# Kernel tuning notes

Hardware: AMD Instinct MI355X
Metric: run time of the kernel (lower is better)

## Reference

```python
import jax, jax.numpy as jnp
import numpy as np

D_MODEL = 1024
D_FF = 4096
N_EXPERTS = 8
TOP_K = 2
B, S = 4, 2048


def setup_inputs() -> dict:
    key = jax.random.key(0)
    ks = jax.random.split(key, 8)
    std = 0.02
    x = jax.random.normal(ks[0], (B, S, D_MODEL), dtype=jnp.float32)
    router_w = jax.random.normal(ks[1], (N_EXPERTS, D_MODEL), dtype=jnp.float32) * std
    router_b = jnp.zeros((N_EXPERTS,), dtype=jnp.float32)
    # stacked expert FFN weights (torch Linear layout: [out, in])
    w1 = jax.random.normal(ks[2], (N_EXPERTS, D_FF, D_MODEL), dtype=jnp.float32) * std
    b1 = jnp.zeros((N_EXPERTS, D_FF), dtype=jnp.float32)
    w2 = jax.random.normal(ks[3], (N_EXPERTS, D_MODEL, D_FF), dtype=jnp.float32) * std
    b2 = jnp.zeros((N_EXPERTS, D_MODEL), dtype=jnp.float32)
    return {"x": x, "router_w": router_w, "router_b": router_b,
            "w1": w1, "b1": b1, "w2": w2, "b2": b2}


def reference(x, router_w, router_b, w1, b1, w2, b2):
    Bx, Sx, D = x.shape
    E = router_b.shape[0]
    xf = x.reshape(-1, D)                                  # [T, D]
    logits = xf @ router_w.T + router_b                    # [T, E]
    probs = jax.nn.softmax(logits, axis=-1)
    topk_w, topk_idx = jax.lax.top_k(probs, TOP_K)         # [T, K]
    topk_w = topk_w / jnp.sum(topk_w, axis=-1, keepdims=True)
    # dense per-token/per-expert combine weights (zero for unselected experts)
    onehot = jax.nn.one_hot(topk_idx, E, dtype=xf.dtype)   # [T, K, E]
    w_dense = jnp.einsum('tke,tk->te', onehot, topk_w)     # [T, E]
    out = jnp.zeros_like(xf)
    for e in range(E):  # small fixed loop over experts (unrolled under jit)
        h = jax.nn.gelu(xf @ w1[e].T + b1[e], approximate=False)  # [T, F]
        out = out + w_dense[:, e:e + 1] * (h @ w2[e].T + b2[e])
    return out.reshape(Bx, Sx, D)
```

## Files before the change

### kernel.cpp

```cpp
#include <hip/hip_runtime.h>
#include <stdint.h>

typedef unsigned short u16;
typedef __bf16 bf16x8 __attribute__((ext_vector_type(8)));
typedef float f32x4 __attribute__((ext_vector_type(4)));

#define T_TOK 8192
#define DM    1024
#define DF    4096
#define NE    8
#define BM    128
#define BK    64
#define MAXT  136


__device__ __forceinline__ u16 f2b(float f) {
  union { float f; uint32_t u; } v; v.f = f;
  uint32_t r = (v.u + 0x7FFFu + ((v.u >> 16) & 1u)) >> 16;
  return (u16)r;
}

__device__ __forceinline__ void async16(const void* g, void* l) {
  __builtin_amdgcn_global_load_lds((const __attribute__((address_space(1))) void*)g,
                                   (__attribute__((address_space(3))) void*)l, 16, 0, 0);
}

__device__ __forceinline__ float fast_gelu(float v) {
  float x = v * 0.70710678118654752f;
  float a = fabsf(x);
  float t = __builtin_amdgcn_rcpf(fmaf(0.3275911f, a, 1.0f));
  float p = t * fmaf(t, fmaf(t, fmaf(t, fmaf(t, 1.061405429f, -1.453152027f),
                                     1.421413741f), -0.284496736f), 0.254829592f);
  float e = __expf(-a * a);
  float erf_a = fmaf(-p, e, 1.0f);
  float erf_x = (x < 0.f) ? -erf_a : erf_a;
  return 0.5f * v * (1.0f + erf_x);
}


__global__ __launch_bounds__(256) void router_k(
    const float* __restrict__ x, const float* __restrict__ rw,
    const float* __restrict__ rb, u16* __restrict__ xb,
    float* __restrict__ wsl, int* __restrict__ bucket, int* __restrict__ counts)
{
  int lane = threadIdx.x & 63;
  int t = blockIdx.x * 4 + (threadIdx.x >> 6);
  const float* xp = x + (size_t)t * DM;
  float acc[NE];
#pragma unroll
  for (int e = 0; e < NE; ++e) acc[e] = 0.f;
  for (int i = 0; i < DM / 64; ++i) {
    int idx = i * 64 + lane;
    float xv = xp[idx];
    xb[(size_t)t * DM + idx] = f2b(xv);
#pragma unroll
    for (int e = 0; e < NE; ++e) acc[e] += xv * rw[e * DM + idx];
  }
#pragma unroll
  for (int e = 0; e < NE; ++e) {
#pragma unroll
    for (int off = 32; off >= 1; off >>= 1) acc[e] += __shfl_xor(acc[e], off);
  }
  if (lane == 0) {
    float l[NE];
#pragma unroll
    for (int e = 0; e < NE; ++e) l[e] = acc[e] + rb[e];
    int i1 = 0;
#pragma unroll
    for (int e = 1; e < NE; ++e) if (l[e] > l[i1]) i1 = e;
    int i2 = (i1 == 0) ? 1 : 0;
#pragma unroll
    for (int e = 0; e < NE; ++e) if (e != i1 && l[e] > l[i2]) i2 = e;
    float e2 = expf(l[i2] - l[i1]);
    float wa = 1.f / (1.f + e2);
    wsl[2 * t]     = wa;
    wsl[2 * t + 1] = 1.f - wa;
    int p1 = atomicAdd(&counts[i1], 1); bucket[i1 * T_TOK + p1] = 2 * t;
    int p2 = atomicAdd(&counts[i2], 1); bucket[i2 * T_TOK + p2] = 2 * t + 1;
  }
}


struct alignas(8) U16x4 { u16 x, y, z, w; };

__global__ __launch_bounds__(256) void cvt_k(const float* __restrict__ w,
                                             u16* __restrict__ o)
{
  int i = blockIdx.x * 256 + threadIdx.x;
  float4 v = ((const float4*)w)[i];
  U16x4 u; u.x = f2b(v.x); u.y = f2b(v.y); u.z = f2b(v.z); u.w = f2b(v.w);
  ((U16x4*)o)[i] = u;
}


__global__ void toff_k(const int* __restrict__ counts, int* __restrict__ toff) {
  if (threadIdx.x == 0 && blockIdx.x == 0) {
    int a = 0;
    for (int e = 0; e < NE; ++e) { toff[e] = a; a += (counts[e] + BM - 1) >> 7; }
    toff[NE] = a;
  }
}


__global__ __launch_bounds__(256, 2) void stage1_k(
    const u16* __restrict__ xb, const u16* __restrict__ w1b,
    const float* __restrict__ b1, const int* __restrict__ bucket,
    const int* __restrict__ counts, const int* __restrict__ toff,
    u16* __restrict__ H)
{
  __shared__ __align__(16) u16 sA[BM * BK];
  __shared__ __align__(16) u16 sB[BM * BK];
  __shared__ int sSlot[BM];

  int bid = blockIdx.y * 32 + blockIdx.x;
  int lid = (bid & 7) * ((32 * MAXT) >> 3) + (bid >> 3);
  int fs = lid & 31;
  int tb = lid >> 5;
  if (tb >= toff[NE]) return;
  int e = 0;
#pragma unroll
  for (int q = 1; q < NE; ++q) if (tb >= toff[q]) e = q;
  int ti = tb - toff[e];
  int cnt = counts[e];
  int tid = threadIdx.x;

  if (tid < BM) {
    int r = ti * BM + tid;
    sSlot[tid] = (r < cnt) ? bucket[e * T_TOK + r] : -1;
  }
  __syncthreads();

  int tokA[4];
#pragma unroll
  for (int c = 0; c < 4; ++c) {
    int s = sSlot[c * 32 + (tid >> 3)];
    tokA[c] = (s < 0) ? 0 : (s >> 1);
  }

  const u16* wB = w1b + ((size_t)e * DF + (size_t)fs * 128) * DM;

  int lane = tid & 63, wid = tid >> 6;
  int wm = wid >> 1, wn = wid & 1;
  int l15 = lane & 15;
  int l7  = l15 & 7;
  int rowb = tid >> 3;
  int swz = (((tid & 7) ^ ((tid >> 3) & 7))) * 8;

  f32x4 acc[4][4] = {};

  for (int k0 = 0; k0 < DM; k0 += BK) {
    __syncthreads();
#pragma unroll
    for (int c = 0; c < 4; ++c) {
      async16(xb + (size_t)tokA[c] * DM + k0 + swz, &sA[c * 2048 + tid * 8]);
      async16(wB + (size_t)(c * 32 + rowb) * DM + k0 + swz, &sB[c * 2048 + tid * 8]);
    }
    __syncthreads();
#pragma unroll
    for (int kk = 0; kk < BK; kk += 32) {
      int gbase = (kk >> 3) + (lane >> 4);
      int offE  = ((gbase ^ l7) << 3);
      bf16x8 af[4], bfr[4];
#pragma unroll
      for (int i = 0; i < 4; ++i)
        af[i] = *(const bf16x8*)&sA[(wm * 64 + i * 16 + l15) * BK + offE];
#pragma unroll
      for (int j = 0; j < 4; ++j)
        bfr[j] = *(const bf16x8*)&sB[(wn * 64 + j * 16 + l15) * BK + offE];
#pragma unroll
      for (int i = 0; i < 4; ++i)
#pragma unroll
        for (int j = 0; j < 4; ++j)
          acc[i][j] = __builtin_amdgcn_mfma_f32_16x16x32_bf16(af[i], bfr[j], acc[i][j], 0, 0, 0);
    }
  }

  int fbase = fs * 128;
#pragma unroll
  for (int i = 0; i < 4; ++i) {
    int mb = wm * 64 + i * 16 + (lane >> 4) * 4;
#pragma unroll
    for (int j = 0; j < 4; ++j) {
      int col = wn * 64 + j * 16 + l15;
      float bias = b1[e * DF + fbase + col];
#pragma unroll
      for (int r = 0; r < 4; ++r) {
        int slot = sSlot[mb + r];
        if (slot >= 0) {
          float v = acc[i][j][r] + bias;
          H[(size_t)slot * DF + fbase + col] = f2b(fast_gelu(v));
        }
      }
    }
  }
}


__global__ __launch_bounds__(256, 2) void stage2_k(
    const u16* __restrict__ H, const u16* __restrict__ w2b,
    const float* __restrict__ b2, const float* __restrict__ wsl,
    const int* __restrict__ bucket, const int* __restrict__ counts,
    const int* __restrict__ toff, float* __restrict__ out)
{
  __shared__ __align__(16) u16 sA[BM * BK];
  __shared__ __align__(16) u16 sB[BM * BK];
  __shared__ int sSlot[BM];

  int bid = blockIdx.y * 8 + blockIdx.x;
  int lid = (bid & 7) * MAXT + (bid >> 3);
  int ds = lid & 7;
  int tb = lid >> 3;
  if (tb >= toff[NE]) return;
  int e = 0;
#pragma unroll
  for (int q = 1; q < NE; ++q) if (tb >= toff[q]) e = q;
  int ti = tb - toff[e];
  int cnt = counts[e];
  int tid = threadIdx.x;

  if (tid < BM) {
    int r = ti * BM + tid;
    sSlot[tid] = (r < cnt) ? bucket[e * T_TOK + r] : -1;
  }
  __syncthreads();

  int rowA[4];
#pragma unroll
  for (int c = 0; c < 4; ++c) {
    int s = sSlot[c * 32 + (tid >> 3)];
    rowA[c] = (s < 0) ? 0 : s;
  }

  const u16* wB = w2b + ((size_t)e * DM + (size_t)ds * 128) * DF;

  int lane = tid & 63, wid = tid >> 6;
  int wm = wid >> 1, wn = wid & 1;
  int l15 = lane & 15;
  int l7  = l15 & 7;
  int rowb = tid >> 3;
  int swz = (((tid & 7) ^ ((tid >> 3) & 7))) * 8;

  f32x4 acc[4][4] = {};

  for (int k0 = 0; k0 < DF; k0 += BK) {
    __syncthreads();
#pragma unroll
    for (int c = 0; c < 4; ++c) {
      async16(H + (size_t)rowA[c] * DF + k0 + swz, &sA[c * 2048 + tid * 8]);
      async16(wB + (size_t)(c * 32 + rowb) * DF + k0 + swz, &sB[c * 2048 + tid * 8]);
    }
    __syncthreads();
#pragma unroll
    for (int kk = 0; kk < BK; kk += 32) {
      int gbase = (kk >> 3) + (lane >> 4);
      int offE  = ((gbase ^ l7) << 3);
      bf16x8 af[4], bfr[4];
#pragma unroll
      for (int i = 0; i < 4; ++i)
        af[i] = *(const bf16x8*)&sA[(wm * 64 + i * 16 + l15) * BK + offE];
#pragma unroll
      for (int j = 0; j < 4; ++j)
        bfr[j] = *(const bf16x8*)&sB[(wn * 64 + j * 16 + l15) * BK + offE];
#pragma unroll
      for (int i = 0; i < 4; ++i)
#pragma unroll
        for (int j = 0; j < 4; ++j)
          acc[i][j] = __builtin_amdgcn_mfma_f32_16x16x32_bf16(af[i], bfr[j], acc[i][j], 0, 0, 0);
    }
  }

  int dbase = ds * 128;
#pragma unroll
  for (int i = 0; i < 4; ++i) {
    int mb = wm * 64 + i * 16 + (lane >> 4) * 4;
#pragma unroll
    for (int j = 0; j < 4; ++j) {
      int col = wn * 64 + j * 16 + l15;
      float bias = b2[e * DM + dbase + col];
#pragma unroll
      for (int r = 0; r < 4; ++r) {
        int slot = sSlot[mb + r];
        if (slot >= 0) {
          float v = (acc[i][j][r] + bias) * wsl[slot];
          atomicAdd(&out[(size_t)(slot >> 1) * DM + dbase + col], v);
        }
      }
    }
  }
}


extern "C" void kernel_launch(void* const* d_in, const int* in_sizes, int n_in,
                              void* d_out, int out_size, void* d_ws, size_t ws_size,
                              hipStream_t stream) {
  const float* x  = (const float*)d_in[0];
  const float* rw = (const float*)d_in[1];
  const float* rb = (const float*)d_in[2];
  const float* w1 = (const float*)d_in[3];
  const float* b1 = (const float*)d_in[4];
  const float* w2 = (const float*)d_in[5];
  const float* b2 = (const float*)d_in[6];
  float* out = (float*)d_out;

  char* ws = (char*)d_ws;
  size_t off = 0;
  auto alloc = [&](size_t bytes) -> void* {
    void* p = ws + off;
    off = (off + bytes + 255) & ~(size_t)255;
    return p;
  };
  u16*   xb     = (u16*)alloc((size_t)T_TOK * DM * 2);
  u16*   w1b    = (u16*)alloc((size_t)NE * DF * DM * 2);
  u16*   w2b    = (u16*)alloc((size_t)NE * DM * DF * 2);
  u16*   H      = (u16*)alloc((size_t)(2 * T_TOK) * DF * 2);
  float* wsl    = (float*)alloc((size_t)(2 * T_TOK) * 4);
  int*   bucket = (int*)alloc((size_t)NE * T_TOK * 4);
  int*   counts = (int*)alloc(256);
  int*   toff   = (int*)alloc(256);

  hipMemsetAsync(counts, 0, NE * sizeof(int), stream);
  hipMemsetAsync(out, 0, (size_t)out_size * sizeof(float), stream);

  router_k<<<T_TOK / 4, 256, 0, stream>>>(x, rw, rb, xb, wsl, bucket, counts);
  cvt_k<<<(NE * DF * DM) / (256 * 4), 256, 0, stream>>>(w1, w1b);
  cvt_k<<<(NE * DM * DF) / (256 * 4), 256, 0, stream>>>(w2, w2b);
  toff_k<<<1, 64, 0, stream>>>(counts, toff);
  stage1_k<<<dim3(DF / 128, MAXT), 256, 0, stream>>>(xb, w1b, b1, bucket, counts, toff, H);
  stage2_k<<<dim3(DM / 128, MAXT), 256, 0, stream>>>(H, w2b, b2, wsl, bucket, counts, toff, out);
}
```

Baseline: 974.3 us.

## Rewrite expert GEMMs as 256x256 double-buffered pipelined tiles with split-K stage2

```diff
diff --git a/kernel.cpp b/kernel.cpp
--- a/kernel.cpp
+++ b/kernel.cpp
@@ -9,9 +9,10 @@
 #define DM    1024
 #define DF    4096
 #define NE    8
-#define BM    128
+#define BM2   256
 #define BK    64
-#define MAXT  136
+#define BUFE  (BM2*BK)
+#define MAXT2 72
 
 
 __device__ __forceinline__ u16 f2b(float f) {
@@ -96,26 +97,134 @@
 __global__ void toff_k(const int* __restrict__ counts, int* __restrict__ toff) {
   if (threadIdx.x == 0 && blockIdx.x == 0) {
     int a = 0;
-    for (int e = 0; e < NE; ++e) { toff[e] = a; a += (counts[e] + BM - 1) >> 7; }
+    for (int e = 0; e < NE; ++e) { toff[e] = a; a += (counts[e] + BM2 - 1) >> 8; }
     toff[NE] = a;
   }
 }
 
 
-__global__ __launch_bounds__(256, 2) void stage1_k(
+#define STG_A(buf,h,p0,p1,koff) do{ \
+  async16((p0) + (koff), sA + (buf)*BUFE + ((h)*128)*BK + tid*8); \
+  async16((p1) + (koff), sA + (buf)*BUFE + ((h)*128+64)*BK + tid*8); }while(0)
+
+#define STG_B(buf,h,koff) do{ \
+  async16(bb + (size_t)((h)*128)*KD + (koff), sB + (buf)*BUFE + ((h)*128)*BK + tid*8); \
+  async16(bb + (size_t)((h)*128+64)*KD + (koff), sB + (buf)*BUFE + ((h)*128+64)*BK + tid*8); }while(0)
+
+#define LD_A(buf,hb) do{ \
+  _Pragma("unroll") for (int m = 0; m < 4; ++m) { \
+    int row_ = wm*128 + (hb)*64 + m*16 + l15; \
+    const u16* base_ = sA + (buf)*BUFE + row_*BK; \
+    _Pragma("unroll") for (int kk = 0; kk < 2; ++kk) \
+      af[m*2+kk] = *(const bf16x8*)(base_ + (((kk*4+ch) ^ (row_ & 7)) << 3)); \
+  } }while(0)
+
+#define LD_B(buf,nh) do{ \
+  _Pragma("unroll") for (int n = 0; n < 2; ++n) { \
+    int row_ = wn*64 + ((nh)*2+n)*16 + l15; \
+    const u16* base_ = sB + (buf)*BUFE + row_*BK; \
+    _Pragma("unroll") for (int kk = 0; kk < 2; ++kk) \
+      bf[((nh)*2+n)*2+kk] = *(const bf16x8*)(base_ + (((kk*4+ch) ^ (row_ & 7)) << 3)); \
+  } }while(0)
+
+#define MM(mh,nh) do{ \
+  _Pragma("unroll") for (int m = 0; m < 4; ++m) \
+  _Pragma("unroll") for (int n = 0; n < 2; ++n) { \
+    f32x4 c_ = acc[(mh)*4+m][(nh)*2+n]; \
+    c_ = __builtin_amdgcn_mfma_f32_16x16x32_bf16(af[m*2+0], bf[((nh)*2+n)*2+0], c_, 0,0,0); \
+    c_ = __builtin_amdgcn_mfma_f32_16x16x32_bf16(af[m*2+1], bf[((nh)*2+n)*2+1], c_, 0,0,0); \
+    acc[(mh)*4+m][(nh)*2+n] = c_; } }while(0)
+
+#define PH_MID() do{ __builtin_amdgcn_s_barrier(); \
+  asm volatile("s_waitcnt lgkmcnt(0)":::"memory"); \
+  __builtin_amdgcn_sched_barrier(0); \
+  __builtin_amdgcn_s_setprio(1); }while(0)
+
+#define PH_END() do{ __builtin_amdgcn_s_setprio(0); \
+  __builtin_amdgcn_s_barrier(); }while(0)
+
+#define PH_END_VM4() do{ __builtin_amdgcn_s_setprio(0); \
+  asm volatile("s_waitcnt vmcnt(4)":::"memory"); \
+  __builtin_amdgcn_sched_barrier(0); \
+  __builtin_amdgcn_s_barrier(); }while(0)
+
+#define PH_END_VM0() do{ __builtin_amdgcn_s_setprio(0); \
+  asm volatile("s_waitcnt vmcnt(0)":::"memory"); \
+  __builtin_amdgcn_sched_barrier(0); \
+  __builtin_amdgcn_s_barrier(); }while(0)
+
+template<int KD, int NITER>
+__device__ __forceinline__ void gemm8(
+    u16* sA, u16* sB,
+    const u16* a0, const u16* a1, const u16* a2, const u16* a3,
+    const u16* bb, int tid, f32x4 (&acc)[8][4])
+{
+  const int lane = tid & 63;
+  const int wid  = tid >> 6;
+  const int wm = wid >> 2, wn = wid & 3;
+  const int l15 = lane & 15;
+  const int ch  = lane >> 4;
+  bf16x8 af[8], bf[8];
+
+  STG_A(0,0,a0,a1,0); STG_A(0,1,a2,a3,0);
+  STG_B(0,0,0);       STG_B(0,1,0);
+  STG_B(1,0,64);      STG_B(1,1,64);
+  asm volatile("s_waitcnt vmcnt(4)":::"memory");
+  __builtin_amdgcn_sched_barrier(0);
+  __builtin_amdgcn_s_barrier();
+
+#pragma unroll 1
+  for (int t = 0; t < NITER - 1; ++t) {
+    LD_A(0,0); LD_B(0,0); STG_A(1,0,a0,a1,64);
+    PH_MID(); MM(0,0); PH_END();
+    LD_B(0,1); STG_A(1,1,a2,a3,64);
+    PH_MID(); MM(0,1); PH_END();
+    LD_A(0,1); STG_B(0,0,128);
+    PH_MID(); MM(1,0); PH_END();
+    STG_B(0,1,128);
+    PH_MID(); MM(1,1); PH_END_VM4();
+    LD_A(1,0); LD_B(1,0); STG_A(0,0,a0,a1,128);
+    PH_MID(); MM(0,0); PH_END();
+    LD_B(1,1); STG_A(0,1,a2,a3,128);
+    PH_MID(); MM(0,1); PH_END();
+    LD_A(1,1); STG_B(1,0,192);
+    PH_MID(); MM(1,0); PH_END();
+    STG_B(1,1,192);
+    PH_MID(); MM(1,1); PH_END_VM4();
+    a0 += 2*BK; a1 += 2*BK; a2 += 2*BK; a3 += 2*BK; bb += 2*BK;
+  }
+  LD_A(0,0); LD_B(0,0); STG_A(1,0,a0,a1,64);
+  PH_MID(); MM(0,0); PH_END();
+  LD_B(0,1); STG_A(1,1,a2,a3,64);
+  PH_MID(); MM(0,1); PH_END();
+  LD_A(0,1);
+  PH_MID(); MM(1,0); PH_END();
+  PH_MID(); MM(1,1); PH_END_VM0();
+  LD_A(1,0); LD_B(1,0);
+  PH_MID(); MM(0,0); PH_END();
+  LD_B(1,1);
+  PH_MID(); MM(0,1); PH_END();
+  LD_A(1,1);
+  PH_MID(); MM(1,0); PH_END();
+  PH_MID(); MM(1,1);
+  __builtin_amdgcn_s_setprio(0);
+}
+
+
+__global__ __launch_bounds__(512, 2) void stage1_k(
     const u16* __restrict__ xb, const u16* __restrict__ w1b,
     const float* __restrict__ b1, const int* __restrict__ bucket,
     const int* __restrict__ counts, const int* __restrict__ toff,
     u16* __restrict__ H)
 {
-  __shared__ __align__(16) u16 sA[BM * BK];
-  __shared__ __align__(16) u16 sB[BM * BK];
-  __shared__ int sSlot[BM];
-
-  int bid = blockIdx.y * 32 + blockIdx.x;
-  int lid = (bid & 7) * ((32 * MAXT) >> 3) + (bid >> 3);
-  int fs = lid & 31;
-  int tb = lid >> 5;
+  __shared__ __align__(16) u16 sA[2*BUFE];
+  __shared__ __align__(16) u16 sB[2*BUFE];
+  __shared__ int sSlot[BM2];
+
+  int bid = blockIdx.y * 16 + blockIdx.x;
+  int lid = (bid & 7) * (16 * MAXT2 / 8) + (bid >> 3);
+  int fs = lid & 15;
+  int tb = lid >> 4;
   if (tb >= toff[NE]) return;
   int e = 0;
 #pragma unroll
@@ -124,70 +233,41 @@
   int cnt = counts[e];
   int tid = threadIdx.x;
 
-  if (tid < BM) {
-    int r = ti * BM + tid;
+  if (tid < BM2) {
+    int r = ti * BM2 + tid;
     sSlot[tid] = (r < cnt) ? bucket[e * T_TOK + r] : -1;
   }
   __syncthreads();
 
-  int tokA[4];
-#pragma unroll
-  for (int c = 0; c < 4; ++c) {
-    int s = sSlot[c * 32 + (tid >> 3)];
-    tokA[c] = (s < 0) ? 0 : (s >> 1);
-  }
-
-  const u16* wB = w1b + ((size_t)e * DF + (size_t)fs * 128) * DM;
+  int rowb = tid >> 3;
+  int swz  = ((tid & 7) ^ (rowb & 7)) * 8;
+  int s0 = sSlot[0*64 + rowb], s1 = sSlot[1*64 + rowb];
+  int s2 = sSlot[2*64 + rowb], s3 = sSlot[3*64 + rowb];
+  const u16* a0 = xb + (size_t)((s0 < 0) ? 0 : (s0 >> 1)) * DM + swz;
+  const u16* a1 = xb + (size_t)((s1 < 0) ? 0 : (s1 >> 1)) * DM + swz;
+  const u16* a2 = xb + (size_t)((s2 < 0) ? 0 : (s2 >> 1)) * DM + swz;
+  const u16* a3 = xb + (size_t)((s3 < 0) ? 0 : (s3 >> 1)) * DM + swz;
+  const u16* bb = w1b + ((size_t)e * DF + (size_t)fs * 256 + rowb) * DM + swz;
+
+  f32x4 acc[8][4] = {};
+  gemm8<DM, DM / BK / 2>(sA, sB, a0, a1, a2, a3, bb, tid, acc);
 
   int lane = tid & 63, wid = tid >> 6;
-  int wm = wid >> 1, wn = wid & 1;
-  int l15 = lane & 15;
-  int l7  = l15 & 7;
-  int rowb = tid >> 3;
-  int swz = (((tid & 7) ^ ((tid >> 3) & 7))) * 8;
-
-  f32x4 acc[4][4] = {};
-
-  for (int k0 = 0; k0 < DM; k0 += BK) {
-    __syncthreads();
-#pragma unroll
-    for (int c = 0; c < 4; ++c) {
-      async16(xb + (size_t)tokA[c] * DM + k0 + swz, &sA[c * 2048 + tid * 8]);
-      async16(wB + (size_t)(c * 32 + rowb) * DM + k0 + swz, &sB[c * 2048 + tid * 8]);
-    }
-    __syncthreads();
-#pragma unroll
-    for (int kk = 0; kk < BK; kk += 32) {
-      int gbase = (kk >> 3) + (lane >> 4);
-      int offE  = ((gbase ^ l7) << 3);
-      bf16x8 af[4], bfr[4];
-#pragma unroll
-      for (int i = 0; i < 4; ++i)
-        af[i] = *(const bf16x8*)&sA[(wm * 64 + i * 16 + l15) * BK + offE];
-#pragma unroll
-      for (int j = 0; j < 4; ++j)
-        bfr[j] = *(const bf16x8*)&sB[(wn * 64 + j * 16 + l15) * BK + offE];
-#pragma unroll
-      for (int i = 0; i < 4; ++i)
-#pragma unroll
-        for (int j = 0; j < 4; ++j)
-          acc[i][j] = __builtin_amdgcn_mfma_f32_16x16x32_bf16(af[i], bfr[j], acc[i][j], 0, 0, 0);
-    }
-  }
-
-  int fbase = fs * 128;
-#pragma unroll
-  for (int i = 0; i < 4; ++i) {
-    int mb = wm * 64 + i * 16 + (lane >> 4) * 4;
-#pragma unroll
-    for (int j = 0; j < 4; ++j) {
-      int col = wn * 64 + j * 16 + l15;
+  int wm = wid >> 2, wn = wid & 3;
+  int l15 = lane & 15, ch = lane >> 4;
+  int fbase = fs * 256;
+#pragma unroll
+  for (int m = 0; m < 8; ++m) {
+    int mb = wm*128 + m*16 + ch*4;
+#pragma unroll
+    for (int n = 0; n < 4; ++n) {
+      int col = wn*64 + n*16 + l15;
       float bias = b1[e * DF + fbase + col];
 #pragma unroll
       for (int r = 0; r < 4; ++r) {
         int slot = sSlot[mb + r];
         if (slot >= 0) {
-          float v = acc[i][j][r] + bias;
+          float v = acc[m][n][r] + bias;
           H[(size_t)slot * DF + fbase + col] = f2b(fast_gelu(v));
         }
       }
@@ -196,20 +276,21 @@
 }
 
 
-__global__ __launch_bounds__(256, 2) void stage2_k(
+__global__ __launch_bounds__(512, 2) void stage2_k(
     const u16* __restrict__ H, const u16* __restrict__ w2b,
     const float* __restrict__ b2, const float* __restrict__ wsl,
     const int* __restrict__ bucket, const int* __restrict__ counts,
     const int* __restrict__ toff, float* __restrict__ out)
 {
-  __shared__ __align__(16) u16 sA[BM * BK];
-  __shared__ __align__(16) u16 sB[BM * BK];
-  __shared__ int sSlot[BM];
+  __shared__ __align__(16) u16 sA[2*BUFE];
+  __shared__ __align__(16) u16 sB[2*BUFE];
+  __shared__ int sSlot[BM2];
 
   int bid = blockIdx.y * 8 + blockIdx.x;
-  int lid = (bid & 7) * MAXT + (bid >> 3);
-  int ds = lid & 7;
+  int lid = (bid & 7) * (8 * MAXT2 / 8) + (bid >> 3);
+  int xx = lid & 7;
   int tb = lid >> 3;
+  int sl = xx & 3, sp = xx >> 2;
   if (tb >= toff[NE]) return;
   int e = 0;
 #pragma unroll
@@ -218,70 +299,42 @@
   int cnt = counts[e];
   int tid = threadIdx.x;
 
-  if (tid < BM) {
-    int r = ti * BM + tid;
+  if (tid < BM2) {
+    int r = ti * BM2 + tid;
     sSlot[tid] = (r < cnt) ? bucket[e * T_TOK + r] : -1;
   }
   __syncthreads();
 
-  int rowA[4];
-#pragma unroll
-  for (int c = 0; c < 4; ++c) {
-    int s = sSlot[c * 32 + (tid >> 3)];
-    rowA[c] = (s < 0) ? 0 : s;
-  }
-
-  const u16* wB = w2b + ((size_t)e * DM + (size_t)ds * 128) * DF;
+  int rowb = tid >> 3;
+  int swz  = ((tid & 7) ^ (rowb & 7)) * 8;
+  int kbase = sp * 2048;
+  int s0 = sSlot[0*64 + rowb], s1 = sSlot[1*64 + rowb];
+  int s2 = sSlot[2*64 + rowb], s3 = sSlot[3*64 + rowb];
+  const u16* a0 = H + (size_t)((s0 < 0) ? 0 : s0) * DF + kbase + swz;
+  const u16* a1 = H + (size_t)((s1 < 0) ? 0 : s1) * DF + kbase + swz;
+  const u16* a2 = H + (size_t)((s2 < 0) ? 0 : s2) * DF + kbase + swz;
+  const u16* a3 = H + (size_t)((s3 < 0) ? 0 : s3) * DF + kbase + swz;
+  const u16* bb = w2b + ((size_t)e * DM + (size_t)sl * 256 + rowb) * DF + kbase + swz;
+
+  f32x4 acc[8][4] = {};
+  gemm8<DF, 2048 / BK / 2>(sA, sB, a0, a1, a2, a3, bb, tid, acc);
 
   int lane = tid & 63, wid = tid >> 6;
-  int wm = wid >> 1, wn = wid & 1;
-  int l15 = lane & 15;
-  int l7  = l15 & 7;
-  int rowb = tid >> 3;
-  int swz = (((tid & 7) ^ ((tid >> 3) & 7))) * 8;
-
-  f32x4 acc[4][4] = {};
-
-  for (int k0 = 0; k0 < DF; k0 += BK) {
-    __syncthreads();
-#pragma unroll
-    for (int c = 0; c < 4; ++c) {
-      async16(H + (size_t)rowA[c] * DF + k0 + swz, &sA[c * 2048 + tid * 8]);
-      async16(wB + (size_t)(c * 32 + rowb) * DF + k0 + swz, &sB[c * 2048 + tid * 8]);
-    }
-    __syncthreads();
-#pragma unroll
-    for (int kk = 0; kk < BK; kk += 32) {
-      int gbase = (kk >> 3) + (lane >> 4);
-      int offE  = ((gbase ^ l7) << 3);
-      bf16x8 af[4], bfr[4];
-#pragma unroll
-      for (int i = 0; i < 4; ++i)
-        af[i] = *(const bf16x8*)&sA[(wm * 64 + i * 16 + l15) * BK + offE];
-#pragma unroll
-      for (int j = 0; j < 4; ++j)
-        bfr[j] = *(const bf16x8*)&sB[(wn * 64 + j * 16 + l15) * BK + offE];
-#pragma unroll
-      for (int i = 0; i < 4; ++i)
-#pragma unroll
-        for (int j = 0; j < 4; ++j)
-          acc[i][j] = __builtin_amdgcn_mfma_f32_16x16x32_bf16(af[i], bfr[j], acc[i][j], 0, 0, 0);
-    }
-  }
-
-  int dbase = ds * 128;
-#pragma unroll
-  for (int i = 0; i < 4; ++i) {
-    int mb = wm * 64 + i * 16 + (lane >> 4) * 4;
-#pragma unroll
-    for (int j = 0; j < 4; ++j) {
-      int col = wn * 64 + j * 16 + l15;
-      float bias = b2[e * DM + dbase + col];
+  int wm = wid >> 2, wn = wid & 3;
+  int l15 = lane & 15, ch = lane >> 4;
+  int dbase = sl * 256;
+#pragma unroll
+  for (int m = 0; m < 8; ++m) {
+    int mb = wm*128 + m*16 + ch*4;
+#pragma unroll
+    for (int n = 0; n < 4; ++n) {
+      int col = wn*64 + n*16 + l15;
+      float bias = (sp == 0) ? b2[e * DM + dbase + col] : 0.f;
 #pragma unroll
       for (int r = 0; r < 4; ++r) {
         int slot = sSlot[mb + r];
         if (slot >= 0) {
-          float v = (acc[i][j][r] + bias) * wsl[slot];
+          float v = (acc[m][n][r] + bias) * wsl[slot];
           atomicAdd(&out[(size_t)(slot >> 1) * DM + dbase + col], v);
         }
       }
@@ -325,6 +378,6 @@
   cvt_k<<<(NE * DF * DM) / (256 * 4), 256, 0, stream>>>(w1, w1b);
   cvt_k<<<(NE * DM * DF) / (256 * 4), 256, 0, stream>>>(w2, w2b);
   toff_k<<<1, 64, 0, stream>>>(counts, toff);
-  stage1_k<<<dim3(DF / 128, MAXT), 256, 0, stream>>>(xb, w1b, b1, bucket, counts, toff, H);
-  stage2_k<<<dim3(DM / 128, MAXT), 256, 0, stream>>>(H, w2b, b2, wsl, bucket, counts, toff, out);
-}
+  stage1_k<<<dim3(DF / 256, MAXT2), 512, 0, stream>>>(xb, w1b, b1, bucket, counts, toff, H);
+  stage2_k<<<dim3(8, MAXT2), 512, 0, stream>>>(H, w2b, b2, wsl, bucket, counts, toff, out);
+}
```

Measured after the change: 1.167 ms. 19.7% more time.

## Double-buffer LDS tiles in both expert GEMMs and grid-stride weight conversion

Applied to the files above, without the earlier changes.

```diff
diff --git a/kernel.cpp b/kernel.cpp
--- a/kernel.cpp
+++ b/kernel.cpp
@@ -11,6 +11,7 @@
 #define NE    8
 #define BM    128
 #define BK    64
+#define TILEE (BM*BK)
 #define MAXT  136
 
 
@@ -84,12 +85,14 @@
 struct alignas(8) U16x4 { u16 x, y, z, w; };
 
 __global__ __launch_bounds__(256) void cvt_k(const float* __restrict__ w,
-                                             u16* __restrict__ o)
+                                             u16* __restrict__ o, int n4)
 {
-  int i = blockIdx.x * 256 + threadIdx.x;
-  float4 v = ((const float4*)w)[i];
-  U16x4 u; u.x = f2b(v.x); u.y = f2b(v.y); u.z = f2b(v.z); u.w = f2b(v.w);
-  ((U16x4*)o)[i] = u;
+  int stride = gridDim.x * 256;
+  for (int i = blockIdx.x * 256 + threadIdx.x; i < n4; i += stride) {
+    float4 v = ((const float4*)w)[i];
+    U16x4 u; u.x = f2b(v.x); u.y = f2b(v.y); u.z = f2b(v.z); u.w = f2b(v.w);
+    ((U16x4*)o)[i] = u;
+  }
 }
 
 
@@ -100,6 +103,42 @@
     toff[NE] = a;
   }
 }
+
+
+#define STG(buf, k0) do{ \
+  async16(aptr0 + (k0), &sA[(buf)*TILEE + 0*2048 + tid*8]); \
+  async16(aptr1 + (k0), &sA[(buf)*TILEE + 1*2048 + tid*8]); \
+  async16(aptr2 + (k0), &sA[(buf)*TILEE + 2*2048 + tid*8]); \
+  async16(aptr3 + (k0), &sA[(buf)*TILEE + 3*2048 + tid*8]); \
+  _Pragma("unroll") for (int c = 0; c < 4; ++c) \
+    async16(bptr + (size_t)(c*32+rowb)*KD + (k0), &sB[(buf)*TILEE + c*2048 + tid*8]); \
+  }while(0)
+
+#define CMP(buf) do{ \
+  _Pragma("unroll") for (int kk = 0; kk < BK; kk += 32) { \
+    int gbase = (kk >> 3) + (lane >> 4); \
+    int offE  = ((gbase ^ l7) << 3); \
+    bf16x8 af[4], bfr[4]; \
+    _Pragma("unroll") for (int i = 0; i < 4; ++i) \
+      af[i] = *(const bf16x8*)&sA[(buf)*TILEE + (wm*64 + i*16 + l15)*BK + offE]; \
+    _Pragma("unroll") for (int j = 0; j < 4; ++j) \
+      bfr[j] = *(const bf16x8*)&sB[(buf)*TILEE + (wn*64 + j*16 + l15)*BK + offE]; \
+    _Pragma("unroll") for (int i = 0; i < 4; ++i) \
+    _Pragma("unroll") for (int j = 0; j < 4; ++j) \
+      acc[i][j] = __builtin_amdgcn_mfma_f32_16x16x32_bf16(af[i], bfr[j], acc[i][j], 0, 0, 0); \
+  } }while(0)
+
+#define KLOOP(KD_, NT_) do{ \
+  const int KD = KD_; \
+  STG(0, 0); \
+  __syncthreads(); \
+  _Pragma("unroll 1") for (int t = 0; t < (NT_)/2 - 1; ++t) { \
+    int k0 = (2*t+1)*BK; \
+    STG(1, k0);      CMP(0); __syncthreads(); \
+    STG(0, k0+BK);   CMP(1); __syncthreads(); \
+  } \
+  STG(1, ((NT_)-1)*BK); CMP(0); __syncthreads(); \
+  CMP(1); }while(0)
 
 
 __global__ __launch_bounds__(256, 2) void stage1_k(
@@ -108,8 +147,8 @@
     const int* __restrict__ counts, const int* __restrict__ toff,
     u16* __restrict__ H)
 {
-  __shared__ __align__(16) u16 sA[BM * BK];
-  __shared__ __align__(16) u16 sB[BM * BK];
+  __shared__ __align__(16) u16 sA[2*TILEE];
+  __shared__ __align__(16) u16 sB[2*TILEE];
   __shared__ int sSlot[BM];
 
   int bid = blockIdx.y * 32 + blockIdx.x;
@@ -130,50 +169,23 @@
   }
   __syncthreads();
 
-  int tokA[4];
-#pragma unroll
-  for (int c = 0; c < 4; ++c) {
-    int s = sSlot[c * 32 + (tid >> 3)];
-    tokA[c] = (s < 0) ? 0 : (s >> 1);
-  }
-
-  const u16* wB = w1b + ((size_t)e * DF + (size_t)fs * 128) * DM;
-
   int lane = tid & 63, wid = tid >> 6;
   int wm = wid >> 1, wn = wid & 1;
   int l15 = lane & 15;
   int l7  = l15 & 7;
   int rowb = tid >> 3;
-  int swz = (((tid & 7) ^ ((tid >> 3) & 7))) * 8;
+  int swz = ((tid & 7) ^ (rowb & 7)) * 8;
+
+  int s0 = sSlot[0*32 + rowb], s1 = sSlot[1*32 + rowb];
+  int s2 = sSlot[2*32 + rowb], s3 = sSlot[3*32 + rowb];
+  const u16* aptr0 = xb + (size_t)((s0 < 0) ? 0 : (s0 >> 1)) * DM + swz;
+  const u16* aptr1 = xb + (size_t)((s1 < 0) ? 0 : (s1 >> 1)) * DM + swz;
+  const u16* aptr2 = xb + (size_t)((s2 < 0) ? 0 : (s2 >> 1)) * DM + swz;
+  const u16* aptr3 = xb + (size_t)((s3 < 0) ? 0 : (s3 >> 1)) * DM + swz;
+  const u16* bptr  = w1b + ((size_t)e * DF + (size_t)fs * 128) * DM + swz;
 
   f32x4 acc[4][4] = {};
-
-  for (int k0 = 0; k0 < DM; k0 += BK) {
-    __syncthreads();
-#pragma unroll
-    for (int c = 0; c < 4; ++c) {
-      async16(xb + (size_t)tokA[c] * DM + k0 + swz, &sA[c * 2048 + tid * 8]);
-      async16(wB + (size_t)(c * 32 + rowb) * DM + k0 + swz, &sB[c * 2048 + tid * 8]);
-    }
-    __syncthreads();
-#pragma unroll
-    for (int kk = 0; kk < BK; kk += 32) {
-      int gbase = (kk >> 3) + (lane >> 4);
-      int offE  = ((gbase ^ l7) << 3);
-      bf16x8 af[4], bfr[4];
-#pragma unroll
-      for (int i = 0; i < 4; ++i)
-        af[i] = *(const bf16x8*)&sA[(wm * 64 + i * 16 + l15) * BK + offE];
-#pragma unroll
-      for (int j = 0; j < 4; ++j)
-        bfr[j] = *(const bf16x8*)&sB[(wn * 64 + j * 16 + l15) * BK + offE];
-#pragma unroll
-      for (int i = 0; i < 4; ++i)
-#pragma unroll
-        for (int j = 0; j < 4; ++j)
-          acc[i][j] = __builtin_amdgcn_mfma_f32_16x16x32_bf16(af[i], bfr[j], acc[i][j], 0, 0, 0);
-    }
-  }
+  KLOOP(DM, DM / BK);
 
   int fbase = fs * 128;
 #pragma unroll
@@ -202,8 +214,8 @@
     const int* __restrict__ bucket, const int* __restrict__ counts,
     const int* __restrict__ toff, float* __restrict__ out)
 {
-  __shared__ __align__(16) u16 sA[BM * BK];
-  __shared__ __align__(16) u16 sB[BM * BK];
+  __shared__ __align__(16) u16 sA[2*TILEE];
+  __shared__ __align__(16) u16 sB[2*TILEE];
   __shared__ int sSlot[BM];
 
   int bid = blockIdx.y * 8 + blockIdx.x;
@@ -224,50 +236,23 @@
   }
   __syncthreads();
 
-  int rowA[4];
-#pragma unroll
-  for (int c = 0; c < 4; ++c) {
-    int s = sSlot[c * 32 + (tid >> 3)];
-    rowA[c] = (s < 0) ? 0 : s;
-  }
-
-  const u16* wB = w2b + ((size_t)e * DM + (size_t)ds * 128) * DF;
-
   int lane = tid & 63, wid = tid >> 6;
   int wm = wid >> 1, wn = wid & 1;
   int l15 = lane & 15;
   int l7  = l15 & 7;
   int rowb = tid >> 3;
-  int swz = (((tid & 7) ^ ((tid >> 3) & 7))) * 8;
+  int swz = ((tid & 7) ^ (rowb & 7)) * 8;
+
+  int s0 = sSlot[0*32 + rowb], s1 = sSlot[1*32 + rowb];
+  int s2 = sSlot[2*32 + rowb], s3 = sSlot[3*32 + rowb];
+  const u16* aptr0 = H + (size_t)((s0 < 0) ? 0 : s0) * DF + swz;
+  const u16* aptr1 = H + (size_t)((s1 < 0) ? 0 : s1) * DF + swz;
+  const u16* aptr2 = H + (size_t)((s2 < 0) ? 0 : s2) * DF + swz;
+  const u16* aptr3 = H + (size_t)((s3 < 0) ? 0 : s3) * DF + swz;
+  const u16* bptr  = w2b + ((size_t)e * DM + (size_t)ds * 128) * DF + swz;
 
   f32x4 acc[4][4] = {};
-
-  for (int k0 = 0; k0 < DF; k0 += BK) {
-    __syncthreads();
-#pragma unroll
-    for (int c = 0; c < 4; ++c) {
-      async16(H + (size_t)rowA[c] * DF + k0 + swz, &sA[c * 2048 + tid * 8]);
-      async16(wB + (size_t)(c * 32 + rowb) * DF + k0 + swz, &sB[c * 2048 + tid * 8]);
-    }
-    __syncthreads();
-#pragma unroll
-    for (int kk = 0; kk < BK; kk += 32) {
-      int gbase = (kk >> 3) + (lane >> 4);
-      int offE  = ((gbase ^ l7) << 3);
-      bf16x8 af[4], bfr[4];
-#pragma unroll
-      for (int i = 0; i < 4; ++i)
-        af[i] = *(const bf16x8*)&sA[(wm * 64 + i * 16 + l15) * BK + offE];
-#pragma unroll
-      for (int j = 0; j < 4; ++j)
-        bfr[j] = *(const bf16x8*)&sB[(wn * 64 + j * 16 + l15) * BK + offE];
-#pragma unroll
-      for (int i = 0; i < 4; ++i)
-#pragma unroll
-        for (int j = 0; j < 4; ++j)
-          acc[i][j] = __builtin_amdgcn_mfma_f32_16x16x32_bf16(af[i], bfr[j], acc[i][j], 0, 0, 0);
-    }
-  }
+  KLOOP(DF, DF / BK);
 
   int dbase = ds * 128;
 #pragma unroll
@@ -322,8 +307,8 @@
   hipMemsetAsync(out, 0, (size_t)out_size * sizeof(float), stream);
 
   router_k<<<T_TOK / 4, 256, 0, stream>>>(x, rw, rb, xb, wsl, bucket, counts);
-  cvt_k<<<(NE * DF * DM) / (256 * 4), 256, 0, stream>>>(w1, w1b);
-  cvt_k<<<(NE * DM * DF) / (256 * 4), 256, 0, stream>>>(w2, w2b);
+  cvt_k<<<2048, 256, 0, stream>>>(w1, w1b, (NE * DF * DM) / 4);
+  cvt_k<<<2048, 256, 0, stream>>>(w2, w2b, (NE * DM * DF) / 4);
   toff_k<<<1, 64, 0, stream>>>(counts, toff);
   stage1_k<<<dim3(DF / 128, MAXT), 256, 0, stream>>>(xb, w1b, b1, bucket, counts, toff, H);
   stage2_k<<<dim3(DM / 128, MAXT), 256, 0, stream>>>(H, w2b, b2, wsl, bucket, counts, toff, out);
```

New measurement: 1.165 ms. 1.2x slower.
